# Optimization experiments

Measured on AMD Instinct MI355X. Metric: run time of the kernel, lower is better.

## Reference

```python
import jax, jax.numpy as jnp
import numpy as np

B, P, R_BAR, WIDTH, ADD_WIDTH, KERNEL_WIDTH = 4096, 1024, 64, 1024, 64, 16
NEG_SLOPE = 0.1

def leaky(x):
    return jnp.where(x > 0, x, NEG_SLOPE * x)

def setup_inputs() -> dict:
    key = jax.random.key(0)
    ks = jax.random.split(key, 16)
    s = lambda fan_in: 1.0 / np.sqrt(fan_in)
    return {
        "x": jax.random.normal(ks[0], (B, P), jnp.float32),
        # PCA layer 1: Linear(p -> r_bar), stored [in, out]
        "W_pca": jax.random.normal(ks[1], (P, R_BAR), jnp.float32) * s(P),
        "b_pca": jnp.zeros((R_BAR,), jnp.float32),
        # relu_stack: Linear(r_bar -> width), Linear(width -> width)
        "W1": jax.random.normal(ks[2], (R_BAR, WIDTH), jnp.float32) * s(R_BAR),
        "b1": jnp.zeros((WIDTH,), jnp.float32),
        "W2": jax.random.normal(ks[3], (WIDTH, WIDTH), jnp.float32) * s(WIDTH),
        "b2": jnp.zeros((WIDTH,), jnp.float32),
        # AdditiveLayer 1: r_bar tiny Linears (kernel_width -> add_width), batched [r, in, out]
        "add1_W": jax.random.normal(ks[4], (R_BAR, KERNEL_WIDTH, ADD_WIDTH), jnp.float32) * s(KERNEL_WIDTH),
        "add1_b": jnp.zeros((R_BAR, ADD_WIDTH), jnp.float32),
        "add1_bias": jnp.zeros((1,), jnp.float32),
        # AdditiveLayer 2: r_bar Linears (add_width -> add_width)
        "add2_W": jax.random.normal(ks[5], (R_BAR, ADD_WIDTH, ADD_WIDTH), jnp.float32) * s(ADD_WIDTH),
        "add2_b": jnp.zeros((R_BAR, ADD_WIDTH), jnp.float32),
        "add2_bias": jnp.zeros((1,), jnp.float32),
        # PCA layer 2: Linear(r_bar*add_width -> r_bar)
        "W_pca2": jax.random.normal(ks[6], (R_BAR * ADD_WIDTH, R_BAR), jnp.float32) * s(R_BAR * ADD_WIDTH),
        "b_pca2": jnp.zeros((R_BAR,), jnp.float32),
        # last layer: Linear(r_bar -> 1)
        "W_last": jax.random.normal(ks[7], (R_BAR, 1), jnp.float32) * s(R_BAR),
        "b_last": jnp.zeros((1,), jnp.float32),
    }

def reference(x, W_pca, b_pca, W1, b1, W2, b2,
              add1_W, add1_b, add1_bias,
              add2_W, add2_b, add2_bias,
              W_pca2, b_pca2, W_last, b_last):
    # PcaLayer 1 (cov/trace bookkeeping does not affect the output)
    t = x @ W_pca + b_pca                                   # [B, r_bar]
    # relu_stack (nn_depth = 2)
    h = leaky(t @ W1 + b1)                                   # [B, width]
    h = leaky(h @ W2 + b2)                                   # [B, width]
    # AdditiveLayer 1: modulo-gather kernel_width cols per slot, batched tiny GEMMs
    idx1 = jnp.arange(R_BAR * KERNEL_WIDTH) % h.shape[1]
    g1 = h[:, idx1].reshape(-1, R_BAR, KERNEL_WIDTH)         # [B, r, kw]
    a = jnp.einsum('brk,rko->bro', g1, add1_W) + add1_b      # [B, r, add_w]
    a = leaky(a.reshape(a.shape[0], -1) + add1_bias)         # [B, r*add_w]
    # AdditiveLayer 2: slices are contiguous (mod is identity) -> plain reshape
    g2 = a.reshape(-1, R_BAR, ADD_WIDTH)
    a2 = jnp.einsum('bri,rio->bro', g2, add2_W) + add2_b
    a2 = leaky(a2.reshape(a2.shape[0], -1) + add2_bias)      # [B, r*add_w]
    # PcaLayer 2 + last layer
    t2 = a2 @ W_pca2 + b_pca2                                # [B, r_bar]
    out = (t2 @ W_last + b_last).reshape(-1, 1)              # [B, 1]
    return out
```

## Files before the change

### kernel.cpp

```cpp
#include <hip/hip_runtime.h>

#define NEG_SLOPE 0.1f

__device__ __forceinline__ float leaky(float v) { return v > 0.0f ? v : NEG_SLOPE * v; }

typedef _Float16 h4_t __attribute__((ext_vector_type(4)));
typedef _Float16 h8_t __attribute__((ext_vector_type(8)));
typedef float f32x4 __attribute__((ext_vector_type(4)));

__device__ __forceinline__ unsigned lds_off(const void* p) {
    return (unsigned)(unsigned long long)p;
}

__device__ __forceinline__ void lgkm0() {
    asm volatile("s_waitcnt lgkmcnt(0)" ::: "memory");
    __builtin_amdgcn_sched_barrier(0);
}

__device__ __forceinline__ h4_t tr16(unsigned addr) {
    h4_t d;
    asm volatile("ds_read_b64_tr_b16 %0, %1" : "=v"(d) : "v"(addr) : "memory");
    return d;
}

__global__ __launch_bounds__(256) void prep_weights(const float* __restrict__ W2,
                                                    const float* __restrict__ W1,
                                                    const float* __restrict__ a1W,
                                                    const float* __restrict__ a2W,
                                                    const float* __restrict__ Wp2,
                                                    _Float16* __restrict__ W2T,
                                                    _Float16* __restrict__ W1T,
                                                    _Float16* __restrict__ wpack)
{
    __shared__ float tile[32][33];
    const int b   = blockIdx.x;
    const int tid = threadIdx.x;

    if (b < 1024) {
        const int n0 = (b & 31) * 32, k0 = (b >> 5) * 32;
        const int r = tid >> 3, c4 = (tid & 7) * 4;
        float4 v = *reinterpret_cast<const float4*>(&W2[(size_t)(k0 + r) * 1024 + n0 + c4]);
        tile[r][c4 + 0] = v.x; tile[r][c4 + 1] = v.y;
        tile[r][c4 + 2] = v.z; tile[r][c4 + 3] = v.w;
        __syncthreads();
        h4_t o;
        o[0] = (_Float16)tile[c4 + 0][r]; o[1] = (_Float16)tile[c4 + 1][r];
        o[2] = (_Float16)tile[c4 + 2][r]; o[3] = (_Float16)tile[c4 + 3][r];
        *reinterpret_cast<h4_t*>(&W2T[(size_t)(n0 + r) * 1024 + k0 + c4]) = o;
    } else if (b < 1088) {
        const int b2 = b - 1024;
        const int n0 = (b2 & 31) * 32, k0 = (b2 >> 5) * 32;
        const int r = tid >> 3, c4 = (tid & 7) * 4;
        float4 v = *reinterpret_cast<const float4*>(&W1[(size_t)(k0 + r) * 1024 + n0 + c4]);
        tile[r][c4 + 0] = v.x; tile[r][c4 + 1] = v.y;
        tile[r][c4 + 2] = v.z; tile[r][c4 + 3] = v.w;
        __syncthreads();
        h4_t o;
        o[0] = (_Float16)tile[c4 + 0][r]; o[1] = (_Float16)tile[c4 + 1][r];
        o[2] = (_Float16)tile[c4 + 2][r]; o[3] = (_Float16)tile[c4 + 3][r];
        *reinterpret_cast<h4_t*>(&W1T[(size_t)(n0 + r) * 64 + k0 + c4]) = o;
    } else {
        const int idx = (b - 1088) * 256 + tid;
        if (idx < 589824) {
            const int r = idx / 9216, qq = idx % 9216;
            float v;
            if (qq < 1024) {
                int nt = qq >> 8, rem = qq & 255, l = rem >> 2, j = rem & 3;
                int n = nt * 16 + (l & 15), k = (l >> 4) * 4 + j;
                v = a1W[(size_t)r * 1024 + k * 64 + n];
            } else if (qq < 5120) {
                int p = qq - 1024, kt = p >> 11, u = p & 2047, nt = u >> 9, s = u & 511,
                    l = s >> 3, j = s & 7;
                int n = nt * 16 + (l & 15), k = kt * 32 + (l >> 4) * 8 + j;
                v = a2W[(size_t)r * 4096 + k * 64 + n];
            } else {
                int p = qq - 5120, kt = p >> 11, u = p & 2047, nt = u >> 9, s = u & 511,
                    l = s >> 3, j = s & 7;
                int n = nt * 16 + (l & 15), k = kt * 32 + (l >> 4) * 8 + j;
                v = Wp2[((size_t)r * 64 + k) * 64 + n];
            }
            wpack[idx] = (_Float16)v;
        }
    }
}

__global__ __launch_bounds__(256) void gemm_n64_splitk(const float* __restrict__ A,
                                                       const float* __restrict__ B,
                                                       float* __restrict__ P)
{
    __shared__ alignas(16) float As[32][33];
    __shared__ alignas(16) float Bs[32][64];
    const int tid   = threadIdx.x;
    const int row0  = blockIdx.x * 32;
    const int kbase = blockIdx.y * 128;
    const int r0    = (tid >> 4) * 2;
    const int c0    = (tid & 15) * 4;
    const int am    = tid >> 3;
    const int ak    = (tid & 7) * 4;
    float acc[2][4] = {};

#pragma unroll
    for (int kc = 0; kc < 128; kc += 32) {
        const int k0 = kbase + kc;
        float4 va = *reinterpret_cast<const float4*>(&A[(size_t)(row0 + am) * 1024 + k0 + ak]);
        As[ak + 0][am] = va.x; As[ak + 1][am] = va.y;
        As[ak + 2][am] = va.z; As[ak + 3][am] = va.w;
#pragma unroll
        for (int p = 0; p < 2; ++p) {
            int idx = tid + p * 256;
            int kk  = idx >> 4;
            int nq  = (idx & 15) * 4;
            *reinterpret_cast<float4*>(&Bs[kk][nq]) =
                *reinterpret_cast<const float4*>(&B[(size_t)(k0 + kk) * 64 + nq]);
        }
        __syncthreads();
#pragma unroll
        for (int k = 0; k < 32; ++k) {
            float a0 = As[k][r0], a1 = As[k][r0 + 1];
            float4 bv = *reinterpret_cast<const float4*>(&Bs[k][c0]);
            acc[0][0] = fmaf(a0, bv.x, acc[0][0]); acc[0][1] = fmaf(a0, bv.y, acc[0][1]);
            acc[0][2] = fmaf(a0, bv.z, acc[0][2]); acc[0][3] = fmaf(a0, bv.w, acc[0][3]);
            acc[1][0] = fmaf(a1, bv.x, acc[1][0]); acc[1][1] = fmaf(a1, bv.y, acc[1][1]);
            acc[1][2] = fmaf(a1, bv.z, acc[1][2]); acc[1][3] = fmaf(a1, bv.w, acc[1][3]);
        }
        __syncthreads();
    }
#pragma unroll
    for (int i = 0; i < 2; ++i) {
        float4 o; o.x = acc[i][0]; o.y = acc[i][1]; o.z = acc[i][2]; o.w = acc[i][3];
        *reinterpret_cast<float4*>(
            &P[((size_t)blockIdx.y * 4096 + row0 + r0 + i) * 64 + c0]) = o;
    }
}

__global__ __launch_bounds__(256) void combine_t16(const float* __restrict__ P,
                                                   const float* __restrict__ bias,
                                                   _Float16* __restrict__ t16)
{
    const int idx = blockIdx.x * 256 + threadIdx.x;
    float s = bias[idx & 63];
#pragma unroll
    for (int c = 0; c < 8; ++c)
        s += P[(size_t)c * 262144 + idx];
    t16[idx] = (_Float16)s;
}

__global__ __launch_bounds__(256) void gemm_k64_mfma(const _Float16* __restrict__ A,
                                                     const _Float16* __restrict__ BT,
                                                     const float* __restrict__ bias,
                                                     _Float16* __restrict__ C)
{
    __shared__ alignas(16) _Float16 As[128 * 64];
    __shared__ alignas(16) _Float16 Bs[128 * 64];
    const int tid = threadIdx.x;
    const int l   = tid & 63;
    const int w   = tid >> 6;
    const int wm  = w >> 1;
    const int wn  = w & 1;
    const int bm0 = blockIdx.y * 128;
    const int bn0 = blockIdx.x * 128;
    const int fr  = l & 15;
    const int fg  = l >> 4;
    const int srow  = l >> 3;
    const int sslot = l & 7;

#pragma unroll
    for (int i = 0; i < 4; ++i) {
        const int r0   = w * 32 + i * 8;
        const int rowA = r0 + srow;
        const int slot = sslot ^ (rowA & 7);
        __builtin_amdgcn_global_load_lds(
            (const __attribute__((address_space(1))) void*)&A[(size_t)(bm0 + rowA) * 64 + slot * 8],
            (__attribute__((address_space(3))) void*)&As[r0 * 64], 16, 0, 0);
        __builtin_amdgcn_global_load_lds(
            (const __attribute__((address_space(1))) void*)&BT[(size_t)(bn0 + rowA) * 64 + slot * 8],
            (__attribute__((address_space(3))) void*)&Bs[r0 * 64], 16, 0, 0);
    }
    __syncthreads();

    f32x4 acc[4][4] = {};
#pragma unroll
    for (int ks = 0; ks < 2; ++ks) {
        h8_t af[4], bf[4];
#pragma unroll
        for (int mt = 0; mt < 4; ++mt) {
            int row = wm * 64 + mt * 16 + fr;
            int sg  = ks * 4 + fg;
            af[mt] = *reinterpret_cast<const h8_t*>(&As[row * 64 + ((sg ^ (row & 7)) << 3)]);
        }
#pragma unroll
        for (int nt = 0; nt < 4; ++nt) {
            int row = wn * 64 + nt * 16 + fr;
            int sg  = ks * 4 + fg;
            bf[nt] = *reinterpret_cast<const h8_t*>(&Bs[row * 64 + ((sg ^ (row & 7)) << 3)]);
        }
#pragma unroll
        for (int mt = 0; mt < 4; ++mt)
#pragma unroll
            for (int nt = 0; nt < 4; ++nt)
                acc[mt][nt] = __builtin_amdgcn_mfma_f32_16x16x32_f16(af[mt], bf[nt],
                                                                     acc[mt][nt], 0, 0, 0);
    }

#pragma unroll
    for (int nt = 0; nt < 4; ++nt) {
        const int col = bn0 + wn * 64 + nt * 16 + fr;
        const float bv = bias[col];
#pragma unroll
        for (int mt = 0; mt < 4; ++mt)
#pragma unroll
            for (int rg = 0; rg < 4; ++rg) {
                const int row = bm0 + wm * 64 + mt * 16 + fg * 4 + rg;
                float v = acc[mt][nt][rg] + bv;
                C[(size_t)row * 1024 + col] = (_Float16)fmaxf(v, NEG_SLOPE * v);
            }
    }
}

__global__ __launch_bounds__(256) void gemm_mfma_f16_v2(const _Float16* __restrict__ A,
                                                        const _Float16* __restrict__ BT,
                                                        const float* __restrict__ bias,
                                                        _Float16* __restrict__ h2t)
{
    __shared__ alignas(16) _Float16 As[64 * 64];
    __shared__ alignas(16) _Float16 Bs[128 * 64];
    const int tid = threadIdx.x;
    const int l   = tid & 63;
    const int w   = tid >> 6;
    const int wm  = w >> 1;
    const int wn  = w & 1;
    const int bm0 = blockIdx.y * 64;
    const int bn0 = blockIdx.x * 128;
    const int fr  = l & 15;
    const int fg  = l >> 4;
    const int srow  = l >> 3;
    const int sslot = l & 7;

    f32x4 acc[2][4] = {};

    for (int k0 = 0; k0 < 1024; k0 += 64) {
#pragma unroll
        for (int i = 0; i < 2; ++i) {
            const int r0   = w * 16 + i * 8;
            const int rowA = r0 + srow;
            const int slot = sslot ^ (rowA & 7);
            __builtin_amdgcn_global_load_lds(
                (const __attribute__((address_space(1))) void*)&A[(size_t)(bm0 + rowA) * 1024 + k0 + slot * 8],
                (__attribute__((address_space(3))) void*)&As[r0 * 64], 16, 0, 0);
        }
#pragma unroll
        for (int i = 0; i < 4; ++i) {
            const int r0   = w * 32 + i * 8;
            const int rowB = r0 + srow;
            const int slot = sslot ^ (rowB & 7);
            __builtin_amdgcn_global_load_lds(
                (const __attribute__((address_space(1))) void*)&BT[(size_t)(bn0 + rowB) * 1024 + k0 + slot * 8],
                (__attribute__((address_space(3))) void*)&Bs[r0 * 64], 16, 0, 0);
        }
        __syncthreads();

#pragma unroll
        for (int ks = 0; ks < 2; ++ks) {
            h8_t af[2], bf[4];
#pragma unroll
            for (int mt = 0; mt < 2; ++mt) {
                int row = wm * 32 + mt * 16 + fr;
                int sg  = ks * 4 + fg;
                af[mt] = *reinterpret_cast<const h8_t*>(&As[row * 64 + ((sg ^ (row & 7)) << 3)]);
            }
#pragma unroll
            for (int nt = 0; nt < 4; ++nt) {
                int row = wn * 64 + nt * 16 + fr;
                int sg  = ks * 4 + fg;
                bf[nt] = *reinterpret_cast<const h8_t*>(&Bs[row * 64 + ((sg ^ (row & 7)) << 3)]);
            }
#pragma unroll
            for (int mt = 0; mt < 2; ++mt)
#pragma unroll
                for (int nt = 0; nt < 4; ++nt)
                    acc[mt][nt] = __builtin_amdgcn_mfma_f32_16x16x32_f16(af[mt], bf[nt],
                                                                         acc[mt][nt], 0, 0, 0);
        }
        __syncthreads();
    }

    const int rblk0 = (bm0 >> 4) + wm * 2;
    const int cblk0 = (bn0 >> 4) + wn * 4;
#pragma unroll
    for (int nt = 0; nt < 4; ++nt) {
        const int col = bn0 + wn * 64 + nt * 16 + fr;
        const float bv = bias[col];
#pragma unroll
        for (int mt = 0; mt < 2; ++mt) {
            h4_t pk;
#pragma unroll
            for (int r = 0; r < 4; ++r) {
                float v = acc[mt][nt][r] + bv;
                pk[r] = (_Float16)fmaxf(v, NEG_SLOPE * v);
            }
            *reinterpret_cast<h4_t*>(
                &h2t[(((size_t)(cblk0 + nt) * 256 + rblk0 + mt) * 16 + fr) * 16 + fg * 4]) = pk;
        }
    }
}

#define RCH 4

__global__ __launch_bounds__(256) void fused_tail5(const _Float16* __restrict__ h2t,
                                                   const _Float16* __restrict__ wpack,
                                                   const float* __restrict__ a1b,
                                                   const float* __restrict__ a1bias,
                                                   const float* __restrict__ a2b,
                                                   const float* __restrict__ a2bias,
                                                   float* __restrict__ partials)
{
    __shared__ alignas(16) _Float16 stage[2][11264];
    __shared__ alignas(16) _Float16 act[4][2048];

    const int tid = threadIdx.x;
    const int l = tid & 63, w = tid >> 6;
    const int c = l & 15, q = l >> 4;
    const int row0  = blockIdx.x * 128;
    const int rbase = blockIdx.y * RCH;
    const float b1s = a1bias[0], b2s = a2bias[0];

    const unsigned trl   = l * 8;
    const unsigned abase = lds_off(&act[w][0]);

    float b1v[RCH][4], b2v[RCH][4];
#pragma unroll
    for (int rl = 0; rl < RCH; ++rl)
#pragma unroll
        for (int nt = 0; nt < 4; ++nt) {
            b1v[rl][nt] = a1b[(rbase + rl) * 64 + nt * 16 + c] + b1s;
            b2v[rl][nt] = a2b[(rbase + rl) * 64 + nt * 16 + c] + b2s;
        }

    auto STAGE = [&](int rl, int b) {
        const int r = rbase + rl;
        const _Float16* hsrc = h2t + ((size_t)r * 256 + blockIdx.x * 8) * 256;
        const _Float16* wsrc = wpack + (size_t)r * 9216;
#pragma unroll
        for (int i = 0; i < 6; ++i) {
            const int ch = i * 4 + w;
            if (ch < 22) {
                const _Float16* src = (ch < 4) ? (hsrc + ch * 512) : (wsrc + (ch - 4) * 512);
                __builtin_amdgcn_global_load_lds(
                    (const __attribute__((address_space(1))) void*)(src + l * 8),
                    (__attribute__((address_space(3))) void*)&stage[b][ch * 512], 16, 0, 0);
            }
        }
    };

    STAGE(0, 0);
    __syncthreads();

    f32x4 accT[2][4] = {};
    int cur = 0;

#pragma unroll
    for (int rl = 0; rl < RCH; ++rl) {
        if (rl + 1 < RCH) STAGE(rl + 1, cur ^ 1);

        const _Float16* sp = &stage[cur][0];
        const unsigned sbytes = lds_off(sp);

        h4_t ha0 = tr16(sbytes + (unsigned)(w) * 512 + trl);
        h4_t ha1 = tr16(sbytes + (unsigned)(w + 4) * 512 + trl);
        lgkm0();
        f32x4 pa[2][4];
#pragma unroll
        for (int nt = 0; nt < 4; ++nt) {
            h4_t bf = *reinterpret_cast<const h4_t*>(&sp[2048 + nt * 256 + l * 4]);
            pa[0][nt] = __builtin_amdgcn_mfma_f32_16x16x16f16(ha0, bf, (f32x4){0.f,0.f,0.f,0.f}, 0, 0, 0);
            pa[1][nt] = __builtin_amdgcn_mfma_f32_16x16x16f16(ha1, bf, (f32x4){0.f,0.f,0.f,0.f}, 0, 0, 0);
        }
#pragma unroll
        for (int j = 0; j < 2; ++j)
#pragma unroll
            for (int nt = 0; nt < 4; ++nt) {
                h4_t pk;
#pragma unroll
                for (int rg = 0; rg < 4; ++rg) {
                    float v = pa[j][nt][rg] + b1v[rl][nt];
                    pk[rg] = (_Float16)fmaxf(v, NEG_SLOPE * v);
                }
                const int kk = nt * 16 + c;
                const int hh = (kk >> 2) & 1;
                const int kp = (kk & 3) | ((kk >> 3) << 2);
                *reinterpret_cast<h4_t*>(&act[w][j * 1024 + hh * 512 + kp * 16 + q * 4]) = pk;
            }
        lgkm0();

        h8_t afB[2][2];
#pragma unroll
        for (int j = 0; j < 2; ++j)
#pragma unroll
            for (int kt = 0; kt < 2; ++kt) {
                h4_t lo = tr16(abase + (unsigned)(j * 2048 + kt * 512) + trl);
                h4_t hi = tr16(abase + (unsigned)(j * 2048 + 1024 + kt * 512) + trl);
                afB[j][kt] = __builtin_shufflevector(lo, hi, 0, 1, 2, 3, 4, 5, 6, 7);
            }
        lgkm0();
        f32x4 pb[2][4] = {};
#pragma unroll
        for (int kt = 0; kt < 2; ++kt)
#pragma unroll
            for (int nt = 0; nt < 4; ++nt) {
                h8_t bf = *reinterpret_cast<const h8_t*>(&sp[3072 + kt * 2048 + nt * 512 + l * 8]);
                pb[0][nt] = __builtin_amdgcn_mfma_f32_16x16x32_f16(afB[0][kt], bf, pb[0][nt], 0, 0, 0);
                pb[1][nt] = __builtin_amdgcn_mfma_f32_16x16x32_f16(afB[1][kt], bf, pb[1][nt], 0, 0, 0);
            }
#pragma unroll
        for (int j = 0; j < 2; ++j)
#pragma unroll
            for (int nt = 0; nt < 4; ++nt) {
                h4_t pk;
#pragma unroll
                for (int rg = 0; rg < 4; ++rg) {
                    float v = pb[j][nt][rg] + b2v[rl][nt];
                    pk[rg] = (_Float16)fmaxf(v, NEG_SLOPE * v);
                }
                const int kk = nt * 16 + c;
                const int hh = (kk >> 2) & 1;
                const int kp = (kk & 3) | ((kk >> 3) << 2);
                *reinterpret_cast<h4_t*>(&act[w][j * 1024 + hh * 512 + kp * 16 + q * 4]) = pk;
            }
        lgkm0();

        h8_t afC[2][2];
#pragma unroll
        for (int j = 0; j < 2; ++j)
#pragma unroll
            for (int kt = 0; kt < 2; ++kt) {
                h4_t lo = tr16(abase + (unsigned)(j * 2048 + kt * 512) + trl);
                h4_t hi = tr16(abase + (unsigned)(j * 2048 + 1024 + kt * 512) + trl);
                afC[j][kt] = __builtin_shufflevector(lo, hi, 0, 1, 2, 3, 4, 5, 6, 7);
            }
        lgkm0();
#pragma unroll
        for (int kt = 0; kt < 2; ++kt)
#pragma unroll
            for (int nt = 0; nt < 4; ++nt) {
                h8_t bf = *reinterpret_cast<const h8_t*>(&sp[7168 + kt * 2048 + nt * 512 + l * 8]);
                accT[0][nt] = __builtin_amdgcn_mfma_f32_16x16x32_f16(afC[0][kt], bf, accT[0][nt], 0, 0, 0);
                accT[1][nt] = __builtin_amdgcn_mfma_f32_16x16x32_f16(afC[1][kt], bf, accT[1][nt], 0, 0, 0);
            }

        __syncthreads();
        cur ^= 1;
    }

#pragma unroll
    for (int j = 0; j < 2; ++j)
#pragma unroll
        for (int nt = 0; nt < 4; ++nt)
#pragma unroll
            for (int rg = 0; rg < 4; ++rg)
                partials[((size_t)blockIdx.y * 4096 + row0 + (w + 4 * j) * 16 + q * 4 + rg) * 64
                         + nt * 16 + c] = accT[j][nt][rg];
}

__global__ __launch_bounds__(256) void reduce_out(const float* __restrict__ partials,
                                                  const float* __restrict__ bp2,
                                                  const float* __restrict__ Wl,
                                                  const float* __restrict__ bl,
                                                  float* __restrict__ out)
{
    const int tid = threadIdx.x;
    const int row = blockIdx.x * 4 + (tid >> 6);
    const int col = tid & 63;
    float s = bp2[col];
#pragma unroll
    for (int c = 0; c < 16; ++c)
        s += partials[(size_t)c * 262144 + (size_t)row * 64 + col];
    s *= Wl[col];
    s += __shfl_xor(s, 1);
    s += __shfl_xor(s, 2);
    s += __shfl_xor(s, 4);
    s += __shfl_xor(s, 8);
    s += __shfl_xor(s, 16);
    s += __shfl_xor(s, 32);
    if (col == 0) out[row] = s + bl[0];
}

extern "C" void kernel_launch(void* const* d_in, const int* in_sizes, int n_in,
                              void* d_out, int out_size, void* d_ws, size_t ws_size,
                              hipStream_t stream)
{
    const float* x      = (const float*)d_in[0];
    const float* Wpca   = (const float*)d_in[1];
    const float* bpca   = (const float*)d_in[2];
    const float* W1     = (const float*)d_in[3];
    const float* b1     = (const float*)d_in[4];
    const float* W2     = (const float*)d_in[5];
    const float* b2     = (const float*)d_in[6];
    const float* a1W    = (const float*)d_in[7];
    const float* a1b    = (const float*)d_in[8];
    const float* a1bias = (const float*)d_in[9];
    const float* a2W    = (const float*)d_in[10];
    const float* a2b    = (const float*)d_in[11];
    const float* a2bias = (const float*)d_in[12];
    const float* Wp2    = (const float*)d_in[13];
    const float* bp2    = (const float*)d_in[14];
    const float* Wl     = (const float*)d_in[15];
    const float* bl     = (const float*)d_in[16];
    float* out = (float*)d_out;

    char* wsb = (char*)d_ws;
    _Float16* t16      = (_Float16*)(wsb);
    _Float16* h1h      = (_Float16*)(wsb + (1ull  << 20));
    _Float16* h2t      = (_Float16*)(wsb + (9ull  << 20));
    _Float16* W2T      = (_Float16*)(wsb + (17ull << 20));
    _Float16* wpack    = (_Float16*)(wsb + (19ull << 20));
    _Float16* W1T      = (_Float16*)(wsb + (21ull << 20));
    float*    partials = (float*)   (wsb + (22ull << 20));
    float*    tpart    = (float*)   (wsb + (9ull  << 20));

    prep_weights<<<dim3(3392), 256, 0, stream>>>(W2, W1, a1W, a2W, Wp2, W2T, W1T, wpack);
    gemm_n64_splitk<<<dim3(128, 8), 256, 0, stream>>>(x, Wpca, tpart);
    combine_t16<<<dim3(1024), 256, 0, stream>>>(tpart, bpca, t16);
    gemm_k64_mfma<<<dim3(8, 32), 256, 0, stream>>>(t16, W1T, b1, h1h);
    gemm_mfma_f16_v2<<<dim3(8, 64), 256, 0, stream>>>(h1h, W2T, b2, h2t);
    fused_tail5<<<dim3(32, 16), 256, 0, stream>>>(h2t, wpack, a1b, a1bias,
                                                  a2b, a2bias, partials);
    reduce_out<<<dim3(1024), 256, 0, stream>>>(partials, bp2, Wl, bl, out);
}
```

Measured before the change: 65.10 us.

## Chain tail GEMMs in transposed register form, dropping LDS activation round-trips

```diff
diff --git a/kernel.cpp b/kernel.cpp
--- a/kernel.cpp
+++ b/kernel.cpp
@@ -65,18 +65,18 @@
             const int r = idx / 9216, qq = idx % 9216;
             float v;
             if (qq < 1024) {
-                int nt = qq >> 8, rem = qq & 255, l = rem >> 2, j = rem & 3;
-                int n = nt * 16 + (l & 15), k = (l >> 4) * 4 + j;
+                int fi = qq >> 8, rem = qq & 255, l = rem >> 2, j = rem & 3;
+                int k = (l >> 4) * 4 + j, n = fi * 16 + (l & 15);
                 v = a1W[(size_t)r * 1024 + k * 64 + n];
             } else if (qq < 5120) {
-                int p = qq - 1024, kt = p >> 11, u = p & 2047, nt = u >> 9, s = u & 511,
-                    l = s >> 3, j = s & 7;
-                int n = nt * 16 + (l & 15), k = kt * 32 + (l >> 4) * 8 + j;
+                int p = qq - 1024;
+                int fj = p >> 10, fi = (p >> 8) & 3, rem = p & 255, l = rem >> 2, j = rem & 3;
+                int k = fi * 16 + (l >> 4) * 4 + j, n = fj * 16 + (l & 15);
                 v = a2W[(size_t)r * 4096 + k * 64 + n];
             } else {
-                int p = qq - 5120, kt = p >> 11, u = p & 2047, nt = u >> 9, s = u & 511,
-                    l = s >> 3, j = s & 7;
-                int n = nt * 16 + (l & 15), k = kt * 32 + (l >> 4) * 8 + j;
+                int p = qq - 5120;
+                int gi = p >> 10, fj = (p >> 8) & 3, rem = p & 255, l = rem >> 2, j = rem & 3;
+                int k = fj * 16 + (l >> 4) * 4 + j, n = gi * 16 + (l & 15);
                 v = Wp2[((size_t)r * 64 + k) * 64 + n];
             }
             wpack[idx] = (_Float16)v;
@@ -306,7 +306,7 @@
 
 #define RCH 4
 
-__global__ __launch_bounds__(256) void fused_tail5(const _Float16* __restrict__ h2t,
+__global__ __launch_bounds__(256) void fused_tail6(const _Float16* __restrict__ h2t,
                                                    const _Float16* __restrict__ wpack,
                                                    const float* __restrict__ a1b,
                                                    const float* __restrict__ a1bias,
@@ -315,7 +315,6 @@
                                                    float* __restrict__ partials)
 {
     __shared__ alignas(16) _Float16 stage[2][11264];
-    __shared__ alignas(16) _Float16 act[4][2048];
 
     const int tid = threadIdx.x;
     const int l = tid & 63, w = tid >> 6;
@@ -324,17 +323,7 @@
     const int rbase = blockIdx.y * RCH;
     const float b1s = a1bias[0], b2s = a2bias[0];
 
-    const unsigned trl   = l * 8;
-    const unsigned abase = lds_off(&act[w][0]);
-
-    float b1v[RCH][4], b2v[RCH][4];
-#pragma unroll
-    for (int rl = 0; rl < RCH; ++rl)
-#pragma unroll
-        for (int nt = 0; nt < 4; ++nt) {
-            b1v[rl][nt] = a1b[(rbase + rl) * 64 + nt * 16 + c] + b1s;
-            b2v[rl][nt] = a2b[(rbase + rl) * 64 + nt * 16 + c] + b2s;
-        }
+    const unsigned trl = l * 8;
 
     auto STAGE = [&](int rl, int b) {
         const int r = rbase + rl;
@@ -360,91 +349,66 @@
 
 #pragma unroll
     for (int rl = 0; rl < RCH; ++rl) {
+        const int r = rbase + rl;
         if (rl + 1 < RCH) STAGE(rl + 1, cur ^ 1);
+
+        float4 b1f[4], b2f[4];
+#pragma unroll
+        for (int fi = 0; fi < 4; ++fi) {
+            b1f[fi] = *reinterpret_cast<const float4*>(&a1b[r * 64 + fi * 16 + q * 4]);
+            b2f[fi] = *reinterpret_cast<const float4*>(&a2b[r * 64 + fi * 16 + q * 4]);
+        }
 
         const _Float16* sp = &stage[cur][0];
         const unsigned sbytes = lds_off(sp);
 
-        h4_t ha0 = tr16(sbytes + (unsigned)(w) * 512 + trl);
-        h4_t ha1 = tr16(sbytes + (unsigned)(w + 4) * 512 + trl);
+        h4_t hf0 = tr16(sbytes + (unsigned)w * 512 + trl);
+        h4_t hf1 = tr16(sbytes + (unsigned)(w + 4) * 512 + trl);
         lgkm0();
-        f32x4 pa[2][4];
-#pragma unroll
-        for (int nt = 0; nt < 4; ++nt) {
-            h4_t bf = *reinterpret_cast<const h4_t*>(&sp[2048 + nt * 256 + l * 4]);
-            pa[0][nt] = __builtin_amdgcn_mfma_f32_16x16x16f16(ha0, bf, (f32x4){0.f,0.f,0.f,0.f}, 0, 0, 0);
-            pa[1][nt] = __builtin_amdgcn_mfma_f32_16x16x16f16(ha1, bf, (f32x4){0.f,0.f,0.f,0.f}, 0, 0, 0);
-        }
-#pragma unroll
-        for (int j = 0; j < 2; ++j)
-#pragma unroll
-            for (int nt = 0; nt < 4; ++nt) {
-                h4_t pk;
-#pragma unroll
-                for (int rg = 0; rg < 4; ++rg) {
-                    float v = pa[j][nt][rg] + b1v[rl][nt];
-                    pk[rg] = (_Float16)fmaxf(v, NEG_SLOPE * v);
-                }
-                const int kk = nt * 16 + c;
-                const int hh = (kk >> 2) & 1;
-                const int kp = (kk & 3) | ((kk >> 3) << 2);
-                *reinterpret_cast<h4_t*>(&act[w][j * 1024 + hh * 512 + kp * 16 + q * 4]) = pk;
-            }
-        lgkm0();
-
-        h8_t afB[2][2];
-#pragma unroll
-        for (int j = 0; j < 2; ++j)
-#pragma unroll
-            for (int kt = 0; kt < 2; ++kt) {
-                h4_t lo = tr16(abase + (unsigned)(j * 2048 + kt * 512) + trl);
-                h4_t hi = tr16(abase + (unsigned)(j * 2048 + 1024 + kt * 512) + trl);
-                afB[j][kt] = __builtin_shufflevector(lo, hi, 0, 1, 2, 3, 4, 5, 6, 7);
-            }
-        lgkm0();
-        f32x4 pb[2][4] = {};
-#pragma unroll
-        for (int kt = 0; kt < 2; ++kt)
-#pragma unroll
-            for (int nt = 0; nt < 4; ++nt) {
-                h8_t bf = *reinterpret_cast<const h8_t*>(&sp[3072 + kt * 2048 + nt * 512 + l * 8]);
-                pb[0][nt] = __builtin_amdgcn_mfma_f32_16x16x32_f16(afB[0][kt], bf, pb[0][nt], 0, 0, 0);
-                pb[1][nt] = __builtin_amdgcn_mfma_f32_16x16x32_f16(afB[1][kt], bf, pb[1][nt], 0, 0, 0);
-            }
-#pragma unroll
-        for (int j = 0; j < 2; ++j)
-#pragma unroll
-            for (int nt = 0; nt < 4; ++nt) {
-                h4_t pk;
-#pragma unroll
-                for (int rg = 0; rg < 4; ++rg) {
-                    float v = pb[j][nt][rg] + b2v[rl][nt];
-                    pk[rg] = (_Float16)fmaxf(v, NEG_SLOPE * v);
-                }
-                const int kk = nt * 16 + c;
-                const int hh = (kk >> 2) & 1;
-                const int kp = (kk & 3) | ((kk >> 3) << 2);
-                *reinterpret_cast<h4_t*>(&act[w][j * 1024 + hh * 512 + kp * 16 + q * 4]) = pk;
-            }
-        lgkm0();
-
-        h8_t afC[2][2];
-#pragma unroll
-        for (int j = 0; j < 2; ++j)
-#pragma unroll
-            for (int kt = 0; kt < 2; ++kt) {
-                h4_t lo = tr16(abase + (unsigned)(j * 2048 + kt * 512) + trl);
-                h4_t hi = tr16(abase + (unsigned)(j * 2048 + 1024 + kt * 512) + trl);
-                afC[j][kt] = __builtin_shufflevector(lo, hi, 0, 1, 2, 3, 4, 5, 6, 7);
-            }
-        lgkm0();
-#pragma unroll
-        for (int kt = 0; kt < 2; ++kt)
-#pragma unroll
-            for (int nt = 0; nt < 4; ++nt) {
-                h8_t bf = *reinterpret_cast<const h8_t*>(&sp[7168 + kt * 2048 + nt * 512 + l * 8]);
-                accT[0][nt] = __builtin_amdgcn_mfma_f32_16x16x32_f16(afC[0][kt], bf, accT[0][nt], 0, 0, 0);
-                accT[1][nt] = __builtin_amdgcn_mfma_f32_16x16x32_f16(afC[1][kt], bf, accT[1][nt], 0, 0, 0);
+
+        h4_t aT[2][4];
+#pragma unroll
+        for (int fi = 0; fi < 4; ++fi) {
+            h4_t wf = *reinterpret_cast<const h4_t*>(&sp[2048 + fi * 256 + l * 4]);
+            f32x4 p0 = __builtin_amdgcn_mfma_f32_16x16x16f16(wf, hf0, (f32x4){0.f,0.f,0.f,0.f}, 0, 0, 0);
+            f32x4 p1 = __builtin_amdgcn_mfma_f32_16x16x16f16(wf, hf1, (f32x4){0.f,0.f,0.f,0.f}, 0, 0, 0);
+#pragma unroll
+            for (int rg = 0; rg < 4; ++rg) {
+                float bb = reinterpret_cast<const float*>(&b1f[fi])[rg] + b1s;
+                float v0 = p0[rg] + bb;
+                float v1 = p1[rg] + bb;
+                aT[0][fi][rg] = (_Float16)fmaxf(v0, NEG_SLOPE * v0);
+                aT[1][fi][rg] = (_Float16)fmaxf(v1, NEG_SLOPE * v1);
+            }
+        }
+
+        h4_t a2T[2][4];
+#pragma unroll
+        for (int fj = 0; fj < 4; ++fj) {
+            f32x4 p0 = {0.f,0.f,0.f,0.f}, p1 = {0.f,0.f,0.f,0.f};
+#pragma unroll
+            for (int fi = 0; fi < 4; ++fi) {
+                h4_t wf = *reinterpret_cast<const h4_t*>(&sp[3072 + (fj * 4 + fi) * 256 + l * 4]);
+                p0 = __builtin_amdgcn_mfma_f32_16x16x16f16(wf, aT[0][fi], p0, 0, 0, 0);
+                p1 = __builtin_amdgcn_mfma_f32_16x16x16f16(wf, aT[1][fi], p1, 0, 0, 0);
+            }
+#pragma unroll
+            for (int rg = 0; rg < 4; ++rg) {
+                float bb = reinterpret_cast<const float*>(&b2f[fj])[rg] + b2s;
+                float v0 = p0[rg] + bb;
+                float v1 = p1[rg] + bb;
+                a2T[0][fj][rg] = (_Float16)fmaxf(v0, NEG_SLOPE * v0);
+                a2T[1][fj][rg] = (_Float16)fmaxf(v1, NEG_SLOPE * v1);
+            }
+        }
+
+#pragma unroll
+        for (int gi = 0; gi < 4; ++gi)
+#pragma unroll
+            for (int fj = 0; fj < 4; ++fj) {
+                h4_t wf = *reinterpret_cast<const h4_t*>(&sp[7168 + (gi * 4 + fj) * 256 + l * 4]);
+                accT[0][gi] = __builtin_amdgcn_mfma_f32_16x16x16f16(wf, a2T[0][fj], accT[0][gi], 0, 0, 0);
+                accT[1][gi] = __builtin_amdgcn_mfma_f32_16x16x16f16(wf, a2T[1][fj], accT[1][gi], 0, 0, 0);
             }
 
         __syncthreads();
@@ -452,36 +416,41 @@
     }
 
 #pragma unroll
-    for (int j = 0; j < 2; ++j)
-#pragma unroll
-        for (int nt = 0; nt < 4; ++nt)
+    for (int j = 0; j < 2; ++j) {
+        const int row = row0 + (w + 4 * j) * 16 + c;
+#pragma unroll
+        for (int gi = 0; gi < 4; ++gi)
 #pragma unroll
             for (int rg = 0; rg < 4; ++rg)
-                partials[((size_t)blockIdx.y * 4096 + row0 + (w + 4 * j) * 16 + q * 4 + rg) * 64
-                         + nt * 16 + c] = accT[j][nt][rg];
-}
-
-__global__ __launch_bounds__(256) void reduce_out(const float* __restrict__ partials,
-                                                  const float* __restrict__ bp2,
-                                                  const float* __restrict__ Wl,
-                                                  const float* __restrict__ bl,
-                                                  float* __restrict__ out)
-{
-    const int tid = threadIdx.x;
-    const int row = blockIdx.x * 4 + (tid >> 6);
-    const int col = tid & 63;
-    float s = bp2[col];
-#pragma unroll
-    for (int c = 0; c < 16; ++c)
-        s += partials[(size_t)c * 262144 + (size_t)row * 64 + col];
-    s *= Wl[col];
-    s += __shfl_xor(s, 1);
-    s += __shfl_xor(s, 2);
-    s += __shfl_xor(s, 4);
-    s += __shfl_xor(s, 8);
-    s += __shfl_xor(s, 16);
-    s += __shfl_xor(s, 32);
-    if (col == 0) out[row] = s + bl[0];
+                partials[((size_t)blockIdx.y * 64 + gi * 16 + q * 4 + rg) * 4096 + row] =
+                    accT[j][gi][rg];
+    }
+}
+
+__global__ __launch_bounds__(256) void reduce_out_t(const float* __restrict__ partials,
+                                                    const float* __restrict__ bp2,
+                                                    const float* __restrict__ Wl,
+                                                    const float* __restrict__ bl,
+                                                    float* __restrict__ out)
+{
+    __shared__ float red[4][64];
+    const int tid  = threadIdx.x;
+    const int w    = tid >> 6;
+    const int lane = tid & 63;
+    const int row  = blockIdx.x * 64 + lane;
+    float s = 0.f;
+#pragma unroll
+    for (int f = w * 16; f < w * 16 + 16; ++f) {
+        float v = bp2[f];
+#pragma unroll
+        for (int c = 0; c < 16; ++c)
+            v += partials[((size_t)c * 64 + f) * 4096 + row];
+        s += v * Wl[f];
+    }
+    red[w][lane] = s;
+    __syncthreads();
+    if (w == 0)
+        out[row] = red[0][lane] + red[1][lane] + red[2][lane] + red[3][lane] + bl[0];
 }
 
 extern "C" void kernel_launch(void* const* d_in, const int* in_sizes, int n_in,
@@ -522,7 +491,7 @@
     combine_t16<<<dim3(1024), 256, 0, stream>>>(tpart, bpca, t16);
     gemm_k64_mfma<<<dim3(8, 32), 256, 0, stream>>>(t16, W1T, b1, h1h);
     gemm_mfma_f16_v2<<<dim3(8, 64), 256, 0, stream>>>(h1h, W2T, b2, h2t);
-    fused_tail5<<<dim3(32, 16), 256, 0, stream>>>(h2t, wpack, a1b, a1bias,
+    fused_tail6<<<dim3(32, 16), 256, 0, stream>>>(h2t, wpack, a1b, a1bias,
                                                   a2b, a2bias, partials);
-    reduce_out<<<dim3(1024), 256, 0, stream>>>(partials, bp2, Wl, bl, out);
-}
+    reduce_out_t<<<dim3(64), 256, 0, stream>>>(partials, bp2, Wl, bl, out);
+}
```

New measurement: 68.30 us. 1.05x slower.

## Merge weight prep with split-K PCA GEMM and fuse partial combine into K64 GEMM

Applied to the files above, without the earlier changes.

```diff
diff --git a/kernel.cpp b/kernel.cpp
--- a/kernel.cpp
+++ b/kernel.cpp
@@ -23,16 +23,21 @@
     return d;
 }
 
-__global__ __launch_bounds__(256) void prep_weights(const float* __restrict__ W2,
-                                                    const float* __restrict__ W1,
-                                                    const float* __restrict__ a1W,
-                                                    const float* __restrict__ a2W,
-                                                    const float* __restrict__ Wp2,
-                                                    _Float16* __restrict__ W2T,
-                                                    _Float16* __restrict__ W1T,
-                                                    _Float16* __restrict__ wpack)
+__global__ __launch_bounds__(256) void prep_and_splitk(const float* __restrict__ W2,
+                                                       const float* __restrict__ W1,
+                                                       const float* __restrict__ a1W,
+                                                       const float* __restrict__ a2W,
+                                                       const float* __restrict__ Wp2,
+                                                       const float* __restrict__ x,
+                                                       const float* __restrict__ Wpca,
+                                                       _Float16* __restrict__ W2T,
+                                                       _Float16* __restrict__ W1T,
+                                                       _Float16* __restrict__ wpack,
+                                                       float* __restrict__ P)
 {
     __shared__ float tile[32][33];
+    __shared__ alignas(16) float As[32][33];
+    __shared__ alignas(16) float Bs[32][64];
     const int b   = blockIdx.x;
     const int tid = threadIdx.x;
 
@@ -59,7 +64,7 @@
         o[0] = (_Float16)tile[c4 + 0][r]; o[1] = (_Float16)tile[c4 + 1][r];
         o[2] = (_Float16)tile[c4 + 2][r]; o[3] = (_Float16)tile[c4 + 3][r];
         *reinterpret_cast<h4_t*>(&W1T[(size_t)(n0 + r) * 64 + k0 + c4]) = o;
-    } else {
+    } else if (b < 3392) {
         const int idx = (b - 1088) * 256 + tid;
         if (idx < 589824) {
             const int r = idx / 9216, qq = idx % 9216;
@@ -81,74 +86,56 @@
             }
             wpack[idx] = (_Float16)v;
         }
-    }
-}
-
-__global__ __launch_bounds__(256) void gemm_n64_splitk(const float* __restrict__ A,
-                                                       const float* __restrict__ B,
-                                                       float* __restrict__ P)
-{
-    __shared__ alignas(16) float As[32][33];
-    __shared__ alignas(16) float Bs[32][64];
-    const int tid   = threadIdx.x;
-    const int row0  = blockIdx.x * 32;
-    const int kbase = blockIdx.y * 128;
-    const int r0    = (tid >> 4) * 2;
-    const int c0    = (tid & 15) * 4;
-    const int am    = tid >> 3;
-    const int ak    = (tid & 7) * 4;
-    float acc[2][4] = {};
-
-#pragma unroll
-    for (int kc = 0; kc < 128; kc += 32) {
-        const int k0 = kbase + kc;
-        float4 va = *reinterpret_cast<const float4*>(&A[(size_t)(row0 + am) * 1024 + k0 + ak]);
-        As[ak + 0][am] = va.x; As[ak + 1][am] = va.y;
-        As[ak + 2][am] = va.z; As[ak + 3][am] = va.w;
-#pragma unroll
-        for (int p = 0; p < 2; ++p) {
-            int idx = tid + p * 256;
-            int kk  = idx >> 4;
-            int nq  = (idx & 15) * 4;
-            *reinterpret_cast<float4*>(&Bs[kk][nq]) =
-                *reinterpret_cast<const float4*>(&B[(size_t)(k0 + kk) * 64 + nq]);
-        }
-        __syncthreads();
-#pragma unroll
-        for (int k = 0; k < 32; ++k) {
-            float a0 = As[k][r0], a1 = As[k][r0 + 1];
-            float4 bv = *reinterpret_cast<const float4*>(&Bs[k][c0]);
-            acc[0][0] = fmaf(a0, bv.x, acc[0][0]); acc[0][1] = fmaf(a0, bv.y, acc[0][1]);
-            acc[0][2] = fmaf(a0, bv.z, acc[0][2]); acc[0][3] = fmaf(a0, bv.w, acc[0][3]);
-            acc[1][0] = fmaf(a1, bv.x, acc[1][0]); acc[1][1] = fmaf(a1, bv.y, acc[1][1]);
-            acc[1][2] = fmaf(a1, bv.z, acc[1][2]); acc[1][3] = fmaf(a1, bv.w, acc[1][3]);
-        }
-        __syncthreads();
-    }
-#pragma unroll
-    for (int i = 0; i < 2; ++i) {
-        float4 o; o.x = acc[i][0]; o.y = acc[i][1]; o.z = acc[i][2]; o.w = acc[i][3];
-        *reinterpret_cast<float4*>(
-            &P[((size_t)blockIdx.y * 4096 + row0 + r0 + i) * 64 + c0]) = o;
-    }
-}
-
-__global__ __launch_bounds__(256) void combine_t16(const float* __restrict__ P,
-                                                   const float* __restrict__ bias,
-                                                   _Float16* __restrict__ t16)
-{
-    const int idx = blockIdx.x * 256 + threadIdx.x;
-    float s = bias[idx & 63];
-#pragma unroll
-    for (int c = 0; c < 8; ++c)
-        s += P[(size_t)c * 262144 + idx];
-    t16[idx] = (_Float16)s;
-}
-
-__global__ __launch_bounds__(256) void gemm_k64_mfma(const _Float16* __restrict__ A,
-                                                     const _Float16* __restrict__ BT,
-                                                     const float* __restrict__ bias,
-                                                     _Float16* __restrict__ C)
+    } else {
+        const int b2    = b - 3392;
+        const int row0  = (b2 & 127) * 32;
+        const int kbase = (b2 >> 7) * 128;
+        const int r0    = (tid >> 4) * 2;
+        const int c0    = (tid & 15) * 4;
+        const int am    = tid >> 3;
+        const int ak    = (tid & 7) * 4;
+        float acc[2][4] = {};
+
+#pragma unroll
+        for (int kc = 0; kc < 128; kc += 32) {
+            const int k0 = kbase + kc;
+            float4 va = *reinterpret_cast<const float4*>(&x[(size_t)(row0 + am) * 1024 + k0 + ak]);
+            As[ak + 0][am] = va.x; As[ak + 1][am] = va.y;
+            As[ak + 2][am] = va.z; As[ak + 3][am] = va.w;
+#pragma unroll
+            for (int p = 0; p < 2; ++p) {
+                int idx = tid + p * 256;
+                int kk  = idx >> 4;
+                int nq  = (idx & 15) * 4;
+                *reinterpret_cast<float4*>(&Bs[kk][nq]) =
+                    *reinterpret_cast<const float4*>(&Wpca[(size_t)(k0 + kk) * 64 + nq]);
+            }
+            __syncthreads();
+#pragma unroll
+            for (int k = 0; k < 32; ++k) {
+                float a0 = As[k][r0], a1 = As[k][r0 + 1];
+                float4 bv = *reinterpret_cast<const float4*>(&Bs[k][c0]);
+                acc[0][0] = fmaf(a0, bv.x, acc[0][0]); acc[0][1] = fmaf(a0, bv.y, acc[0][1]);
+                acc[0][2] = fmaf(a0, bv.z, acc[0][2]); acc[0][3] = fmaf(a0, bv.w, acc[0][3]);
+                acc[1][0] = fmaf(a1, bv.x, acc[1][0]); acc[1][1] = fmaf(a1, bv.y, acc[1][1]);
+                acc[1][2] = fmaf(a1, bv.z, acc[1][2]); acc[1][3] = fmaf(a1, bv.w, acc[1][3]);
+            }
+            __syncthreads();
+        }
+#pragma unroll
+        for (int i = 0; i < 2; ++i) {
+            float4 o; o.x = acc[i][0]; o.y = acc[i][1]; o.z = acc[i][2]; o.w = acc[i][3];
+            *reinterpret_cast<float4*>(
+                &P[((size_t)(b2 >> 7) * 4096 + row0 + r0 + i) * 64 + c0]) = o;
+        }
+    }
+}
+
+__global__ __launch_bounds__(256) void gemm_k64_mfma_fused(const float* __restrict__ tpart,
+                                                           const float* __restrict__ bpca,
+                                                           const _Float16* __restrict__ BT,
+                                                           const float* __restrict__ bias,
+                                                           _Float16* __restrict__ C)
 {
     __shared__ alignas(16) _Float16 As[128 * 64];
     __shared__ alignas(16) _Float16 Bs[128 * 64];
@@ -169,9 +156,22 @@
         const int r0   = w * 32 + i * 8;
         const int rowA = r0 + srow;
         const int slot = sslot ^ (rowA & 7);
-        __builtin_amdgcn_global_load_lds(
-            (const __attribute__((address_space(1))) void*)&A[(size_t)(bm0 + rowA) * 64 + slot * 8],
-            (__attribute__((address_space(3))) void*)&As[r0 * 64], 16, 0, 0);
+        const size_t base = (size_t)(bm0 + rowA) * 64 + slot * 8;
+        float4 s0 = *reinterpret_cast<const float4*>(&bpca[slot * 8]);
+        float4 s1 = *reinterpret_cast<const float4*>(&bpca[slot * 8 + 4]);
+#pragma unroll
+        for (int ch = 0; ch < 8; ++ch) {
+            float4 p0 = *reinterpret_cast<const float4*>(&tpart[(size_t)ch * 262144 + base]);
+            float4 p1 = *reinterpret_cast<const float4*>(&tpart[(size_t)ch * 262144 + base + 4]);
+            s0.x += p0.x; s0.y += p0.y; s0.z += p0.z; s0.w += p0.w;
+            s1.x += p1.x; s1.y += p1.y; s1.z += p1.z; s1.w += p1.w;
+        }
+        h8_t av;
+        av[0] = (_Float16)s0.x; av[1] = (_Float16)s0.y;
+        av[2] = (_Float16)s0.z; av[3] = (_Float16)s0.w;
+        av[4] = (_Float16)s1.x; av[5] = (_Float16)s1.y;
+        av[6] = (_Float16)s1.z; av[7] = (_Float16)s1.w;
+        *reinterpret_cast<h8_t*>(&As[r0 * 64 + l * 8]) = av;
         __builtin_amdgcn_global_load_lds(
             (const __attribute__((address_space(1))) void*)&BT[(size_t)(bn0 + rowA) * 64 + slot * 8],
             (__attribute__((address_space(3))) void*)&Bs[r0 * 64], 16, 0, 0);
@@ -508,7 +508,6 @@
     float* out = (float*)d_out;
 
     char* wsb = (char*)d_ws;
-    _Float16* t16      = (_Float16*)(wsb);
     _Float16* h1h      = (_Float16*)(wsb + (1ull  << 20));
     _Float16* h2t      = (_Float16*)(wsb + (9ull  << 20));
     _Float16* W2T      = (_Float16*)(wsb + (17ull << 20));
@@ -517,10 +516,9 @@
     float*    partials = (float*)   (wsb + (22ull << 20));
     float*    tpart    = (float*)   (wsb + (9ull  << 20));
 
-    prep_weights<<<dim3(3392), 256, 0, stream>>>(W2, W1, a1W, a2W, Wp2, W2T, W1T, wpack);
-    gemm_n64_splitk<<<dim3(128, 8), 256, 0, stream>>>(x, Wpca, tpart);
-    combine_t16<<<dim3(1024), 256, 0, stream>>>(tpart, bpca, t16);
-    gemm_k64_mfma<<<dim3(8, 32), 256, 0, stream>>>(t16, W1T, b1, h1h);
+    prep_and_splitk<<<dim3(4416), 256, 0, stream>>>(W2, W1, a1W, a2W, Wp2, x, Wpca,
+                                                    W2T, W1T, wpack, tpart);
+    gemm_k64_mfma_fused<<<dim3(8, 32), 256, 0, stream>>>(tpart, bpca, W1T, b1, h1h);
     gemm_mfma_f16_v2<<<dim3(8, 64), 256, 0, stream>>>(h1h, W2T, b2, h2t);
     fused_tail5<<<dim3(32, 16), 256, 0, stream>>>(h2t, wpack, a1b, a1bias,
                                                   a2b, a2bias, partials);
```

New measurement: 72.89 us. 12.0% more time.
